# Performance work log

Hardware: AMD Instinct MI355X
Metric: run time of the kernel (lower is better)

## Reference

```python
import jax, jax.numpy as jnp
import numpy as np

NUM_POINTS = 100000
BATCH = 4096
K = 10


def setup_inputs() -> dict:
    key = jax.random.key(0)
    k1, k2, k3, k4, k5 = jax.random.split(key, 5)
    rays_o = jax.random.normal(k1, (BATCH, 3), dtype=jnp.float32)
    rays_d = jax.random.normal(k2, (BATCH, 3), dtype=jnp.float32)
    xyz = jax.random.normal(k3, (NUM_POINTS, 3), dtype=jnp.float32) * 0.1
    features_dc = jax.random.normal(k4, (NUM_POINTS, 1, 3), dtype=jnp.float32)
    opacity = jax.random.normal(k5, (NUM_POINTS, 1), dtype=jnp.float32)
    return {"rays_o": rays_o, "rays_d": rays_d, "xyz": xyz,
            "features_dc": features_dc, "opacity": opacity}


def reference(rays_o, rays_d, xyz, features_dc, opacity):
    # colors = sigmoid(features[:,0,:]) ; features[:,0,:] == features_dc[:,0,:]
    colors = jax.nn.sigmoid(features_dc[:, 0, :])          # [N,3]
    op = jax.nn.sigmoid(opacity[:, 0])                      # [N]
    ray_centers = rays_o + rays_d * 3.0                     # [B,3]
    # Euclidean cdist via ||a||^2 + ||b||^2 - 2 a.b (matmul form, like torch.cdist p=2)
    sq = (jnp.sum(ray_centers * ray_centers, axis=1)[:, None]
          + jnp.sum(xyz * xyz, axis=1)[None, :]
          - 2.0 * ray_centers @ xyz.T)                      # [B,N]
    distances = jnp.sqrt(jnp.maximum(sq, 0.0))
    # top-K smallest distances per ray
    _, idx = jax.lax.top_k(-distances, K)                   # [B,K]
    d_sel = jnp.take_along_axis(distances, idx, axis=1)     # [B,K]
    w = jnp.exp(-d_sel * 0.1) * op[idx]                     # [B,K]
    w = w / (jnp.sum(w, axis=1, keepdims=True) + 1e-8)
    rgb = jnp.einsum('bk,bkc->bc', w, colors[idx])          # [B,3]
    return rgb
```

## Files before the change

### kernel.cpp

```cpp
#include <hip/hip_runtime.h>
#include <math.h>

#define NPTS   100000
#define NRAYS  4096
#define KTOP   10
#define KMER   12
#define CAP    128
#define LCAP   12

#define PPAIR  4
#define SBLK   49
#define RCS    64
#define RPBS   (NRAYS / RCS)

#define TPAIR  4
#define NPART  64
#define TRAYS  8
#define TGRP   16

typedef float v2f __attribute__((ext_vector_type(2)));

static_assert(SBLK * 2048 >= NPTS, "scan covers all points");
static_assert(TGRP * 2048 <= NPTS, "theta sample within real points");

__device__ __forceinline__ float4 make_center(const float* __restrict__ ro,
                                              const float* __restrict__ rd,
                                              int ray, float w) {
    float ox = ro[3 * ray + 0], oy = ro[3 * ray + 1], oz = ro[3 * ray + 2];
    float dx = rd[3 * ray + 0], dy = rd[3 * ray + 1], dz = rd[3 * ray + 2];
    float cx, cy, cz;
    {
#pragma clang fp contract(off)
        cx = ox + dx * 3.0f;
        cy = oy + dy * 3.0f;
        cz = oz + dz * 3.0f;
    }
    return make_float4(cx, cy, cz, w);
}

__device__ __forceinline__ float sigm(float x) { return 1.0f / (1.0f + expf(-x)); }

__device__ __forceinline__ unsigned long long mkkey(float sc, int id, bool v) {
    unsigned u = __float_as_uint(sc);
    u = (u & 0x80000000u) ? ~u : (u | 0x80000000u);
    unsigned long long k = ((unsigned long long)u << 32) | (unsigned)(~id);
    return v ? k : 0ull;
}

__global__ __launch_bounds__(256, 2) void theta_kernel(const float* __restrict__ xyz,
                                                       const float* __restrict__ ro,
                                                       const float* __restrict__ rd,
                                                       float* __restrict__ theta,
                                                       int* __restrict__ cnt) {
    __shared__ float4 rsh[TRAYS];
    __shared__ float  Msh[4][TRAYS][64];
    const int tid = threadIdx.x, wave = tid >> 6, lane = tid & 63;
    const int rbase = blockIdx.x * TRAYS;

    if (tid < TRAYS) rsh[tid] = make_center(ro, rd, rbase + tid, 0.0f);
    __syncthreads();

    float4 rr[TRAYS];
#pragma unroll
    for (int r = 0; r < TRAYS; ++r) rr[r] = rsh[r];

    v2f M[TRAYS];
#pragma unroll
    for (int r = 0; r < TRAYS; ++r) M[r] = (v2f){-INFINITY, -INFINITY};

#pragma unroll 1
    for (int g = 0; g < TGRP; g += 2) {
        v2f px[2][TPAIR], py[2][TPAIR], pz[2][TPAIR], pw[2][TPAIR];
#pragma unroll
        for (int h = 0; h < 2; ++h) {
            const int id0 = (g + h) * 2048 + wave * 512 + lane;
#pragma unroll
            for (int u = 0; u < TPAIR; ++u) {
                int ia = id0 + (2 * u) * 64, ib = id0 + (2 * u + 1) * 64;
                float xa = xyz[3 * ia + 0], ya = xyz[3 * ia + 1], za = xyz[3 * ia + 2];
                float xb = xyz[3 * ib + 0], yb = xyz[3 * ib + 1], zb = xyz[3 * ib + 2];
                px[h][u] = (v2f){xa, xb}; py[h][u] = (v2f){ya, yb}; pz[h][u] = (v2f){za, zb};
                pw[h][u] = (v2f){-0.5f * fmaf(xa, xa, fmaf(ya, ya, za * za)),
                                 -0.5f * fmaf(xb, xb, fmaf(yb, yb, zb * zb))};
            }
        }
#pragma unroll
        for (int r = 0; r < TRAYS; ++r) {
            const v2f rx = (v2f){rr[r].x, rr[r].x};
            const v2f ry = (v2f){rr[r].y, rr[r].y};
            const v2f rz = (v2f){rr[r].z, rr[r].z};
            v2f m = M[r];
#pragma unroll
            for (int h = 0; h < 2; ++h) {
#pragma unroll
                for (int u = 0; u < TPAIR; ++u) {
                    v2f t = __builtin_elementwise_fma(pz[h][u], rz, pw[h][u]);
                    t = __builtin_elementwise_fma(py[h][u], ry, t);
                    t = __builtin_elementwise_fma(px[h][u], rx, t);
                    m = __builtin_elementwise_max(m, t);
                }
            }
            M[r] = m;
        }
    }

#pragma unroll
    for (int r = 0; r < TRAYS; ++r)
        Msh[wave][r][lane] = fmaxf(M[r].x, M[r].y);
    __syncthreads();

    if (tid < TRAYS) {
        float vs[KTOP];
#pragma unroll
        for (int j = 0; j < KTOP; ++j) vs[j] = -INFINITY;
#pragma unroll 1
        for (int p = 0; p < NPART; ++p) {
            float v = fmaxf(fmaxf(Msh[0][tid][p], Msh[1][tid][p]),
                            fmaxf(Msh[2][tid][p], Msh[3][tid][p]));
#pragma unroll
            for (int t = KTOP - 1; t >= 1; --t) {
                bool up = v > vs[t - 1], here = v > vs[t];
                vs[t] = up ? vs[t - 1] : (here ? v : vs[t]);
            }
            vs[0] = fmaxf(vs[0], v);
        }
        theta[rbase + tid] = vs[KTOP - 1];
        cnt[rbase + tid] = 0;
    }
}

__global__ __launch_bounds__(256) void scan_kernel(const float* __restrict__ xyz,
                                                   const float* __restrict__ ro,
                                                   const float* __restrict__ rd,
                                                   const float* __restrict__ theta,
                                                   int* __restrict__ cnt,
                                                   float2* __restrict__ cand) {
    __shared__ float4 rsh[RPBS];
    __shared__ int    lcnt[RPBS];
    __shared__ float2 lbuf[RPBS][LCAP];
    const int pblk = blockIdx.x, rchunk = blockIdx.y;
    const int tid = threadIdx.x, wave = tid >> 6, lane = tid & 63;
    const int rbase = rchunk * RPBS;

    if (tid < RPBS) {
        rsh[tid] = make_center(ro, rd, rbase + tid, theta[rbase + tid]);
        lcnt[tid] = 0;
    }

    const int id0 = pblk * 2048 + wave * 512 + lane;
    v2f px[PPAIR], py[PPAIR], pz[PPAIR], pw[PPAIR];
#pragma unroll
    for (int u = 0; u < PPAIR; ++u) {
        int ia = id0 + (2 * u) * 64, ib = id0 + (2 * u + 1) * 64;
        bool va = ia < NPTS, vb = ib < NPTS;
        int ca = va ? ia : 0, cb = vb ? ib : 0;
        float xa = xyz[3 * ca + 0], ya = xyz[3 * ca + 1], za = xyz[3 * ca + 2];
        float xb = xyz[3 * cb + 0], yb = xyz[3 * cb + 1], zb = xyz[3 * cb + 2];
        px[u] = (v2f){xa, xb}; py[u] = (v2f){ya, yb}; pz[u] = (v2f){za, zb};
        pw[u] = (v2f){va ? -0.5f * fmaf(xa, xa, fmaf(ya, ya, za * za)) : -INFINITY,
                      vb ? -0.5f * fmaf(xb, xb, fmaf(yb, yb, zb * zb)) : -INFINITY};
    }
    __syncthreads();

    auto emit = [&](int r, float sc, int id) {
        int slot = atomicAdd(&lcnt[r], 1);
        float2 e = make_float2(sc, __int_as_float(id));
        if (slot < LCAP) lbuf[r][slot] = e;
        else {
            int gs = atomicAdd(&cnt[rbase + r], 1);
            if (gs < CAP) cand[((rbase + r) << 7) + gs] = e;
        }
    };

#pragma unroll 4
    for (int r = 0; r < RPBS; ++r) {
        float4 rp = rsh[r];
        const v2f rx = (v2f){rp.x, rp.x}, ry = (v2f){rp.y, rp.y}, rz = (v2f){rp.z, rp.z};
        v2f s[PPAIR];
        v2f a0, a1;
        {
            v2f t = __builtin_elementwise_fma(pz[0], rz, pw[0]);
            t = __builtin_elementwise_fma(py[0], ry, t);
            t = __builtin_elementwise_fma(px[0], rx, t);
            s[0] = t; a0 = t;
            t = __builtin_elementwise_fma(pz[1], rz, pw[1]);
            t = __builtin_elementwise_fma(py[1], ry, t);
            t = __builtin_elementwise_fma(px[1], rx, t);
            s[1] = t; a1 = t;
            t = __builtin_elementwise_fma(pz[2], rz, pw[2]);
            t = __builtin_elementwise_fma(py[2], ry, t);
            t = __builtin_elementwise_fma(px[2], rx, t);
            s[2] = t; a0 = __builtin_elementwise_max(a0, t);
            t = __builtin_elementwise_fma(pz[3], rz, pw[3]);
            t = __builtin_elementwise_fma(py[3], ry, t);
            t = __builtin_elementwise_fma(px[3], rx, t);
            s[3] = t; a1 = __builtin_elementwise_max(a1, t);
        }
        v2f am = __builtin_elementwise_max(a0, a1);
        float hm = fmaxf(am.x, am.y);

        if (__ballot(hm >= rp.w)) {
#pragma unroll
            for (int u = 0; u < PPAIR; ++u) {
                if (__ballot(s[u].x >= rp.w)) {
                    if (s[u].x >= rp.w) emit(r, s[u].x, id0 + (2 * u) * 64);
                }
                if (__ballot(s[u].y >= rp.w)) {
                    if (s[u].y >= rp.w) emit(r, s[u].y, id0 + (2 * u + 1) * 64);
                }
            }
        }
    }

    __syncthreads();
    if (tid < RPBS) {
        int n = lcnt[tid];
        n = n < LCAP ? n : LCAP;
        if (n > 0) {
            const int rayid = rbase + tid;
            int base = atomicAdd(&cnt[rayid], n);
            for (int j = 0; j < n; ++j) {
                int slot = base + j;
                if (slot < CAP) cand[(rayid << 7) + slot] = lbuf[tid][j];
            }
        }
    }
}

__global__ __launch_bounds__(256) void merge_kernel(const float* __restrict__ ro,
                                                    const float* __restrict__ rd,
                                                    const int* __restrict__ cnt,
                                                    const float2* __restrict__ cand,
                                                    const float* __restrict__ xyz,
                                                    const float* __restrict__ fdc,
                                                    const float* __restrict__ opac,
                                                    float* __restrict__ out) {
    const int wave = threadIdx.x >> 6, lane = threadIdx.x & 63;
    const int ray = blockIdx.x * 4 + wave;

    int n = cnt[ray];
    n = n < CAP ? n : CAP;

    const float2* cl = cand + (ray << 7);
    float2 e0 = cl[lane];
    float2 e1 = cl[64 + lane];
    int id0 = __float_as_int(e0.y), id1 = __float_as_int(e1.y);

    unsigned long long k0 = mkkey(e0.x, id0, lane < n);
    unsigned long long k1 = mkkey(e1.x, id1, lane + 64 < n);

    int sel = -1;
    unsigned long long kl = k0 > k1 ? k0 : k1;
#pragma unroll
    for (int j = 0; j < KMER; ++j) {
        unsigned long long m = kl;
#pragma unroll
        for (int off = 1; off < 64; off <<= 1) {
            unsigned long long o = __shfl_xor(m, off);
            m = m > o ? m : o;
        }
        bool win = (kl == m) && (m != 0ull);
        int wid = (k0 >= k1) ? id0 : id1;
        unsigned long long wmask = __ballot(win);
        int wl = __ffsll(wmask) - 1;
        int bid = __shfl(wid, wl & 63);
        if (m == 0ull) bid = -1;
        if (lane == j) sel = bid;
        if (win) {
            if (k0 >= k1) k0 = 0ull; else k1 = 0ull;
            kl = k0 > k1 ? k0 : k1;
        }
    }

    float ox = ro[3 * ray + 0], oy = ro[3 * ray + 1], oz = ro[3 * ray + 2];
    float dx = rd[3 * ray + 0], dy = rd[3 * ray + 1], dz = rd[3 * ray + 2];
    float cxf, cyf, czf;
    {
#pragma clang fp contract(off)
        cxf = ox + dx * 3.0f;
        cyf = oy + dy * 3.0f;
        czf = oz + dz * 3.0f;
    }
    double Cx = (double)cxf, Cy = (double)cyf, Cz = (double)czf;
    double cn = Cx * Cx + Cy * Cy + Cz * Cz;

    bool valid = (lane < KMER) && (sel >= 0);
    int pid = valid ? sel : 0;
    double X = (double)xyz[3 * pid + 0];
    double Y = (double)xyz[3 * pid + 1];
    double Z = (double)xyz[3 * pid + 2];
    double sq = valid ? (cn + (X * X + Y * Y + Z * Z) - 2.0 * (Cx * X + Cy * Y + Cz * Z))
                      : (double)INFINITY;
    int cid = valid ? sel : 0x7fffffff;

    int rank = 0;
#pragma unroll
    for (int k = 0; k < KMER; ++k) {
        double sk = __shfl(sq, k);
        int    ik = __shfl(cid, k);
        if ((sk < sq) || (sk == sq && ik < cid)) ++rank;
    }

    bool take = valid && (rank < KTOP);
    float w = 0.0f, rr = 0.0f, gg = 0.0f, bb = 0.0f;
    if (take) {
        float dd = sqrtf(fmaxf((float)sq, 0.0f));
        w  = expf(-0.1f * dd) * sigm(opac[pid]);
        rr = w * sigm(fdc[3 * pid + 0]);
        gg = w * sigm(fdc[3 * pid + 1]);
        bb = w * sigm(fdc[3 * pid + 2]);
    }
#pragma unroll
    for (int off = 1; off < 64; off <<= 1) {
        w  += __shfl_xor(w,  off);
        rr += __shfl_xor(rr, off);
        gg += __shfl_xor(gg, off);
        bb += __shfl_xor(bb, off);
    }
    if (lane == 0) {
        float inv = 1.0f / (w + 1e-8f);
        out[3 * ray + 0] = rr * inv;
        out[3 * ray + 1] = gg * inv;
        out[3 * ray + 2] = bb * inv;
    }
}

extern "C" void kernel_launch(void* const* d_in, const int* in_sizes, int n_in,
                              void* d_out, int out_size, void* d_ws, size_t ws_size,
                              hipStream_t stream) {
    const float* rays_o = (const float*)d_in[0];
    const float* rays_d = (const float*)d_in[1];
    const float* xyz    = (const float*)d_in[2];
    const float* fdc    = (const float*)d_in[3];
    const float* opac   = (const float*)d_in[4];
    float* out = (float*)d_out;

    char* w = (char*)d_ws;
    float*  theta  = (float*)w;  w += (size_t)NRAYS * 4;
    int*    cnt    = (int*)w;    w += (size_t)NRAYS * 4;
    float2* cand   = (float2*)w;

    theta_kernel<<<NRAYS / TRAYS, 256, 0, stream>>>(xyz, rays_o, rays_d, theta, cnt);
    scan_kernel<<<dim3(SBLK, RCS), 256, 0, stream>>>(xyz, rays_o, rays_d, theta, cnt, cand);
    merge_kernel<<<NRAYS / 4, 256, 0, stream>>>(rays_o, rays_d, cnt, cand, xyz, fdc, opac, out);
}
```

Baseline: 149.8 us.

## Precompute ray centers with thresholds in theta kernel and stream them into scan

The theta kernel now writes each ray's center and threshold as a float4, so the scan kernel no longer recomputes centers or stages them in LDS. The scan loop loads four ray records at a time from global memory into wave-uniform scalar registers via readfirstlane. It also replaces the per-pair ballot checks with direct per-lane emits, and adds an occupancy hint of 6 blocks per CU. This aims to cut LDS traffic and the startup barrier work, and to reduce branch overhead in the hot loop. The cost is more global (cached) loads per ray and possible register pressure from the launch bound.

```diff
diff --git a/kernel.cpp b/kernel.cpp
--- a/kernel.cpp
+++ b/kernel.cpp
@@ -40,6 +40,17 @@
 
 __device__ __forceinline__ float sigm(float x) { return 1.0f / (1.0f + expf(-x)); }
 
+__device__ __forceinline__ float rfl(float x) {
+    return __int_as_float(__builtin_amdgcn_readfirstlane(__float_as_int(x)));
+}
+
+__device__ __forceinline__ v2f score2(v2f px, v2f py, v2f pz, v2f pw,
+                                      v2f rx, v2f ry, v2f rz) {
+    v2f t = __builtin_elementwise_fma(pz, rz, pw);
+    t = __builtin_elementwise_fma(py, ry, t);
+    return __builtin_elementwise_fma(px, rx, t);
+}
+
 __device__ __forceinline__ unsigned long long mkkey(float sc, int id, bool v) {
     unsigned u = __float_as_uint(sc);
     u = (u & 0x80000000u) ? ~u : (u | 0x80000000u);
@@ -50,7 +61,7 @@
 __global__ __launch_bounds__(256, 2) void theta_kernel(const float* __restrict__ xyz,
                                                        const float* __restrict__ ro,
                                                        const float* __restrict__ rd,
-                                                       float* __restrict__ theta,
+                                                       float4* __restrict__ c4,
                                                        int* __restrict__ cnt) {
     __shared__ float4 rsh[TRAYS];
     __shared__ float  Msh[4][TRAYS][64];
@@ -124,28 +135,24 @@
             }
             vs[0] = fmaxf(vs[0], v);
         }
-        theta[rbase + tid] = vs[KTOP - 1];
+        float4 c = rsh[tid];
+        c.w = vs[KTOP - 1];
+        c4[rbase + tid] = c;
         cnt[rbase + tid] = 0;
     }
 }
 
-__global__ __launch_bounds__(256) void scan_kernel(const float* __restrict__ xyz,
-                                                   const float* __restrict__ ro,
-                                                   const float* __restrict__ rd,
-                                                   const float* __restrict__ theta,
-                                                   int* __restrict__ cnt,
-                                                   float2* __restrict__ cand) {
-    __shared__ float4 rsh[RPBS];
+__global__ __launch_bounds__(256, 6) void scan_kernel(const float* __restrict__ xyz,
+                                                      const float4* __restrict__ c4,
+                                                      int* __restrict__ cnt,
+                                                      float2* __restrict__ cand) {
     __shared__ int    lcnt[RPBS];
     __shared__ float2 lbuf[RPBS][LCAP];
     const int pblk = blockIdx.x, rchunk = blockIdx.y;
     const int tid = threadIdx.x, wave = tid >> 6, lane = tid & 63;
     const int rbase = rchunk * RPBS;
 
-    if (tid < RPBS) {
-        rsh[tid] = make_center(ro, rd, rbase + tid, theta[rbase + tid]);
-        lcnt[tid] = 0;
-    }
+    if (tid < RPBS) lcnt[tid] = 0;
 
     const int id0 = pblk * 2048 + wave * 512 + lane;
     v2f px[PPAIR], py[PPAIR], pz[PPAIR], pw[PPAIR];
@@ -172,42 +179,34 @@
         }
     };
 
-#pragma unroll 4
-    for (int r = 0; r < RPBS; ++r) {
-        float4 rp = rsh[r];
-        const v2f rx = (v2f){rp.x, rp.x}, ry = (v2f){rp.y, rp.y}, rz = (v2f){rp.z, rp.z};
-        v2f s[PPAIR];
-        v2f a0, a1;
-        {
-            v2f t = __builtin_elementwise_fma(pz[0], rz, pw[0]);
-            t = __builtin_elementwise_fma(py[0], ry, t);
-            t = __builtin_elementwise_fma(px[0], rx, t);
-            s[0] = t; a0 = t;
-            t = __builtin_elementwise_fma(pz[1], rz, pw[1]);
-            t = __builtin_elementwise_fma(py[1], ry, t);
-            t = __builtin_elementwise_fma(px[1], rx, t);
-            s[1] = t; a1 = t;
-            t = __builtin_elementwise_fma(pz[2], rz, pw[2]);
-            t = __builtin_elementwise_fma(py[2], ry, t);
-            t = __builtin_elementwise_fma(px[2], rx, t);
-            s[2] = t; a0 = __builtin_elementwise_max(a0, t);
-            t = __builtin_elementwise_fma(pz[3], rz, pw[3]);
-            t = __builtin_elementwise_fma(py[3], ry, t);
-            t = __builtin_elementwise_fma(px[3], rx, t);
-            s[3] = t; a1 = __builtin_elementwise_max(a1, t);
-        }
-        v2f am = __builtin_elementwise_max(a0, a1);
-        float hm = fmaxf(am.x, am.y);
-
-        if (__ballot(hm >= rp.w)) {
-#pragma unroll
-            for (int u = 0; u < PPAIR; ++u) {
-                if (__ballot(s[u].x >= rp.w)) {
-                    if (s[u].x >= rp.w) emit(r, s[u].x, id0 + (2 * u) * 64);
-                }
-                if (__ballot(s[u].y >= rp.w)) {
-                    if (s[u].y >= rp.w) emit(r, s[u].y, id0 + (2 * u + 1) * 64);
-                }
+#pragma unroll 1
+    for (int rb = 0; rb < RPBS; rb += 4) {
+        float4 q[4];
+#pragma unroll
+        for (int j = 0; j < 4; ++j) q[j] = c4[rbase + rb + j];
+#pragma unroll
+        for (int j = 0; j < 4; ++j) {
+            const float cx = rfl(q[j].x), cy = rfl(q[j].y);
+            const float cz = rfl(q[j].z), th = rfl(q[j].w);
+            const v2f rx = (v2f){cx, cx}, ry = (v2f){cy, cy}, rz = (v2f){cz, cz};
+            v2f t0 = score2(px[0], py[0], pz[0], pw[0], rx, ry, rz);
+            v2f t1 = score2(px[1], py[1], pz[1], pw[1], rx, ry, rz);
+            v2f t2 = score2(px[2], py[2], pz[2], pw[2], rx, ry, rz);
+            v2f t3 = score2(px[3], py[3], pz[3], pw[3], rx, ry, rz);
+            v2f am = __builtin_elementwise_max(__builtin_elementwise_max(t0, t1),
+                                               __builtin_elementwise_max(t2, t3));
+            float hm = fmaxf(am.x, am.y);
+
+            if (__ballot(hm >= th)) {
+                const int r = rb + j;
+                if (t0.x >= th) emit(r, t0.x, id0 + 0 * 64);
+                if (t0.y >= th) emit(r, t0.y, id0 + 1 * 64);
+                if (t1.x >= th) emit(r, t1.x, id0 + 2 * 64);
+                if (t1.y >= th) emit(r, t1.y, id0 + 3 * 64);
+                if (t2.x >= th) emit(r, t2.x, id0 + 4 * 64);
+                if (t2.y >= th) emit(r, t2.y, id0 + 5 * 64);
+                if (t3.x >= th) emit(r, t3.x, id0 + 6 * 64);
+                if (t3.y >= th) emit(r, t3.y, id0 + 7 * 64);
             }
         }
     }
@@ -336,11 +335,11 @@
     float* out = (float*)d_out;
 
     char* w = (char*)d_ws;
-    float*  theta  = (float*)w;  w += (size_t)NRAYS * 4;
-    int*    cnt    = (int*)w;    w += (size_t)NRAYS * 4;
-    float2* cand   = (float2*)w;
-
-    theta_kernel<<<NRAYS / TRAYS, 256, 0, stream>>>(xyz, rays_o, rays_d, theta, cnt);
-    scan_kernel<<<dim3(SBLK, RCS), 256, 0, stream>>>(xyz, rays_o, rays_d, theta, cnt, cand);
+    float4* c4   = (float4*)w;   w += (size_t)NRAYS * 16;
+    int*    cnt  = (int*)w;      w += (size_t)NRAYS * 4;
+    float2* cand = (float2*)w;
+
+    theta_kernel<<<NRAYS / TRAYS, 256, 0, stream>>>(xyz, rays_o, rays_d, c4, cnt);
+    scan_kernel<<<dim3(SBLK, RCS), 256, 0, stream>>>(xyz, c4, cnt, cand);
     merge_kernel<<<NRAYS / 4, 256, 0, stream>>>(rays_o, rays_d, cnt, cand, xyz, fdc, opac, out);
 }
```

Result: slower. 154.4 us (+3.1%).
